# Performance work log

Measured on AMD Instinct MI355X. Metric: run time of the kernel, lower is better.

## Reference

```python
import jax, jax.numpy as jnp
import numpy as np

C = 256
CI = C // 2  # inter_channels


def conv1x1(x, w, b):
    # x: [B,C,H,W], w: [O,C], b: [O] -> [B,O,H,W]
    return jnp.einsum('bchw,oc->bohw', x, w) + b[None, :, None, None]


def setup_inputs() -> dict:
    key = jax.random.key(0)
    ks = jax.random.split(key, 9)
    B, H, W = 8, 56, 56
    s = 0.02
    return {
        'x': jax.random.normal(ks[0], (B, C, H, W), dtype=jnp.float32),
        'g_w': jax.random.normal(ks[1], (CI, C), dtype=jnp.float32) * s,
        'g_b': jax.random.normal(ks[2], (CI,), dtype=jnp.float32) * s,
        'theta_w': jax.random.normal(ks[3], (CI, C), dtype=jnp.float32) * s,
        'theta_b': jax.random.normal(ks[4], (CI,), dtype=jnp.float32) * s,
        'phi_w': jax.random.normal(ks[5], (CI, C), dtype=jnp.float32) * s,
        'phi_b': jax.random.normal(ks[6], (CI,), dtype=jnp.float32) * s,
        'W_w': jax.random.normal(ks[7], (C, CI), dtype=jnp.float32) * s,
        'W_b': jax.random.normal(ks[8], (C,), dtype=jnp.float32) * s,
    }


def reference(x, g_w, g_b, theta_w, theta_b, phi_w, phi_b, W_w, W_b):
    B, Cc, H, Wd = x.shape
    N = H * Wd
    g_x = conv1x1(x, g_w, g_b).reshape(B, CI, N).transpose(0, 2, 1)        # [B,N,CI]
    theta_x = conv1x1(x, theta_w, theta_b).reshape(B, CI, N).transpose(0, 2, 1)  # [B,N,CI]
    phi_x = conv1x1(x, phi_w, phi_b).reshape(B, CI, N)                     # [B,CI,N]
    f = jnp.einsum('bnc,bcm->bnm', theta_x, phi_x)                         # [B,N,N]
    attn = jax.nn.softmax(f, axis=-1)
    y = jnp.einsum('bnm,bmc->bnc', attn, g_x)                              # [B,N,CI]
    y = y.transpose(0, 2, 1).reshape(B, CI, H, Wd)                         # [B,CI,H,W]
    z = conv1x1(y, W_w, W_b) + x
    return z
```

## Files before the change

### kernel.cpp

```cpp
#include <hip/hip_runtime.h>

#define NB 8
#define C 256
#define CI 128
#define NPIX 3136
#define NT 64
#define NTILES 49
#define NGQ 13
#define NROWT 98
#define NSPLIT 4
#define LOG2E 1.44269504f

typedef unsigned short u16;
typedef unsigned int u32;
typedef __bf16 bf16x8 __attribute__((ext_vector_type(8)));
typedef float f32x4 __attribute__((ext_vector_type(4)));
typedef float f32x16 __attribute__((ext_vector_type(16)));

static __device__ __forceinline__ u16 f2b(float f) {
  union { float f; u32 u; } v; v.f = f;
  u32 r = v.u + 0x7FFFu + ((v.u >> 16) & 1u);
  return (u16)(r >> 16);
}
static __device__ __forceinline__ float b2f(u16 v) {
  union { u32 u; float f; } x; x.u = ((u32)v) << 16; return x.f;
}
static __device__ __forceinline__ u32 cvtpk(float lo, float hi) {
  u32 r;
  asm("v_cvt_pk_bf16_f32 %0, %1, %2" : "=v"(r) : "v"(lo), "v"(hi));
  return r;
}
static __device__ __forceinline__ void swap32(u32& x, u32& y) {
  asm("v_permlane32_swap_b32 %0, %1" : "+v"(x), "+v"(y));
}
static __device__ __forceinline__ void gl16(const void* g, void* l) {
  __builtin_amdgcn_global_load_lds(
      (const __attribute__((address_space(1))) u32*)g,
      (__attribute__((address_space(3))) u32*)l, 16, 0, 0);
}

__global__ __launch_bounds__(256) void k0_convert(
    const float* __restrict__ g_w, const float* __restrict__ th_w,
    const float* __restrict__ ph_w, const float* __restrict__ W_w,
    u16* __restrict__ wcat, u16* __restrict__ Wbf) {
  int i = blockIdx.x * 256 + threadIdx.x;
  if (i < 98304) {
    int o = i >> 8, c = i & 255;
    float v = (o < 128) ? g_w[o * 256 + c]
            : (o < 256) ? th_w[(o - 128) * 256 + c] * LOG2E
                        : ph_w[(o - 256) * 256 + c];
    wcat[i] = f2b(v);
  } else {
    int j = i - 98304;
    Wbf[j] = f2b(W_w[j]);
  }
}

__global__ __launch_bounds__(256) void k1_proj(
    const float* __restrict__ x, const float* __restrict__ g_b,
    const float* __restrict__ th_b, const float* __restrict__ ph_b,
    const u16* __restrict__ wcat, u16* __restrict__ thO,
    u16* __restrict__ phO, u16* __restrict__ gO) {
  __shared__ __align__(16) u16 xT[32 * 256];
  char* xTb = reinterpret_cast<char*>(xT);
  int tid = threadIdx.x;
  int b = blockIdx.x / NROWT, nt = blockIdx.x % NROWT;
  int n0 = nt * 32;
  const float* xb = x + (size_t)b * C * NPIX;
  {
    int c0 = tid >> 3, nq = tid & 7;
    for (int k = 0; k < 8; ++k) {
      int c = c0 + 32 * k;
      float4 xv = *reinterpret_cast<const float4*>(xb + (size_t)c * NPIX + n0 + 4 * nq);
      float vals[4] = {xv.x, xv.y, xv.z, xv.w};
#pragma unroll
      for (int j = 0; j < 4; ++j) {
        int row = 4 * nq + j;
        int off = row * 512 + ((((c >> 3) ^ (row & 7))) << 4) + (c & 7) * 2;
        *reinterpret_cast<u16*>(xTb + off) = f2b(vals[j]);
      }
    }
  }
  __syncthreads();
  int wave = tid >> 6, lane = tid & 63;
  int wq = wave & 1, wo = wave >> 1;
  int r = 16 * wq + (lane & 15);
  bf16x8 a[8];
#pragma unroll
  for (int kk = 0; kk < 8; ++kk) {
    int ch = 4 * kk + (lane >> 4);
    a[kk] = *reinterpret_cast<const bf16x8*>(xTb + r * 512 + ((ch ^ (r & 7)) << 4));
  }
  for (int os = 12 * wo; os < 12 * wo + 12; ++os) {
    int o = 16 * os + (lane & 15);
    f32x4 acc = {0.f, 0.f, 0.f, 0.f};
    const u16* wrow = wcat + (size_t)o * 256 + 8 * (lane >> 4);
#pragma unroll
    for (int kk = 0; kk < 8; ++kk) {
      bf16x8 bb = *reinterpret_cast<const bf16x8*>(wrow + 32 * kk);
      acc = __builtin_amdgcn_mfma_f32_16x16x32_bf16(a[kk], bb, acc, 0, 0, 0);
    }
    int p = os >> 3;
    int ol = (os & 7) * 16 + (lane & 15);
    const float* bias = (p == 0) ? g_b : (p == 1) ? th_b : ph_b;
    float bv = bias[ol];
    if (p == 1) bv *= LOG2E;
    int nbase = n0 + 16 * wq + 4 * (lane >> 4);
    if (p == 0) {
      ushort4 pk;
      pk.x = f2b(acc[0] + bv); pk.y = f2b(acc[1] + bv);
      pk.z = f2b(acc[2] + bv); pk.w = f2b(acc[3] + bv);
      *reinterpret_cast<ushort4*>(gO + ((size_t)b * CI + ol) * NPIX + nbase) = pk;
    } else {
      u16* dst = (p == 1) ? thO : phO;
#pragma unroll
      for (int j = 0; j < 4; ++j)
        dst[((size_t)b * NPIX + nbase + j) * CI + ol] = f2b(acc[j] + bv);
    }
  }
}

__global__ __launch_bounds__(512, 2) void k2_attn(
    const u16* __restrict__ th, const u16* __restrict__ ph,
    const u16* __restrict__ gbuf, u16* __restrict__ yp,
    float* __restrict__ lm) {
  __shared__ __align__(16) char lds[65536];
  int tid = threadIdx.x, wave = tid >> 6, lane = tid & 63;
  int h5 = lane >> 5, l31 = lane & 31;
  int bid = blockIdx.x;
  int s = bid & 3, rest = bid >> 2;
  int b = rest / NGQ, ng = rest % NGQ;
  int qbase = ng * 256 + wave * 32;
  if (qbase + 32 > NPIX) qbase = NPIX - 32;
  int ts = (NTILES * s) >> 2, te = (NTILES * (s + 1)) >> 2;

  bf16x8 bth[8];
  {
    const u16* trow = th + ((size_t)b * NPIX + qbase + l31) * CI;
#pragma unroll
    for (int ks = 0; ks < 8; ++ks)
      bth[ks] = *reinterpret_cast<const bf16x8*>(trow + 16 * ks + 8 * h5);
  }
  float lrun = 0.f;
  f32x16 yacc[4];
#pragma unroll
  for (int cb = 0; cb < 4; ++cb)
#pragma unroll
    for (int j = 0; j < 16; ++j) yacc[cb][j] = 0.f;

  auto stage = [&](int buf, int mt) {
    int m0 = mt * NT;
    char* phB = lds + buf * 16384;
    char* gB = lds + 32768 + buf * 16384;
#pragma unroll
    for (int c = 0; c < 2; ++c) {
      int call = wave * 2 + c;
      int o = call * 1024 + lane * 16;
      int row = o >> 8, chl = (o >> 4) & 15;
      int chg = chl ^ (row & 15);
      gl16(ph + ((size_t)(b * NPIX + m0 + row)) * CI + chg * 8, phB + call * 1024);
    }
#pragma unroll
    for (int c = 0; c < 2; ++c) {
      int call = wave * 2 + c;
      int o = call * 1024 + lane * 16;
      int ci = o >> 7, chl = (o >> 4) & 7;
      int chg = chl ^ (ci & 7);
      gl16(gbuf + ((size_t)b * CI + ci) * NPIX + m0 + chg * 8, gB + call * 1024);
    }
  };

  stage(0, ts);
  int cur = 0;
  for (int mt = ts; mt < te; ++mt) {
    bool pre = (mt + 1 < te);
    if (pre) stage(cur ^ 1, mt + 1);
    if (pre) {
      asm volatile("s_waitcnt vmcnt(4)" ::: "memory");
    } else {
      asm volatile("s_waitcnt vmcnt(0)" ::: "memory");
    }
    __builtin_amdgcn_s_barrier();
    __builtin_amdgcn_sched_barrier(0);
    char* phB = lds + cur * 16384;
    char* gB = lds + 32768 + cur * 16384;
    f32x16 sv0, sv1;
#pragma unroll
    for (int j = 0; j < 16; ++j) { sv0[j] = 0.f; sv1[j] = 0.f; }
    __builtin_amdgcn_s_setprio(1);
#pragma unroll
    for (int ks = 0; ks < 8; ++ks) {
      int chk = 2 * ks + h5;
      int off = l31 * 256 + ((chk ^ (l31 & 15)) << 4);
      bf16x8 a0 = *reinterpret_cast<const bf16x8*>(phB + off);
      bf16x8 a1 = *reinterpret_cast<const bf16x8*>(phB + off + 8192);
      sv0 = __builtin_amdgcn_mfma_f32_32x32x16_bf16(a0, bth[ks], sv0, 0, 0, 0);
      sv1 = __builtin_amdgcn_mfma_f32_32x32x16_bf16(a1, bth[ks], sv1, 0, 0, 0);
    }
    __builtin_amdgcn_s_setprio(0);
#pragma unroll
    for (int j = 0; j < 16; ++j) {
      sv0[j] = exp2f(sv0[j]);
      sv1[j] = exp2f(sv1[j]);
    }
    float a0 = 0.f, a1 = 0.f, a2 = 0.f, a3 = 0.f;
#pragma unroll
    for (int i = 0; i < 16; i += 4) {
      a0 += sv0[i] + sv1[i];
      a1 += sv0[i + 1] + sv1[i + 1];
      a2 += sv0[i + 2] + sv1[i + 2];
      a3 += sv0[i + 3] + sv1[i + 3];
    }
    lrun += (a0 + a1) + (a2 + a3);
    u32 pk[2][4][2];
#pragma unroll
    for (int t = 0; t < 4; ++t) {
      pk[0][t][0] = cvtpk(sv0[4 * t], sv0[4 * t + 1]);
      pk[0][t][1] = cvtpk(sv0[4 * t + 2], sv0[4 * t + 3]);
      pk[1][t][0] = cvtpk(sv1[4 * t], sv1[4 * t + 1]);
      pk[1][t][1] = cvtpk(sv1[4 * t + 2], sv1[4 * t + 3]);
    }
    __builtin_amdgcn_s_setprio(1);
#pragma unroll
    for (int ks = 0; ks < 4; ++ks) {
      int m2 = ks >> 1, t0 = 2 * (ks & 1);
      swap32(pk[m2][t0][0], pk[m2][t0 + 1][0]);
      swap32(pk[m2][t0][1], pk[m2][t0 + 1][1]);
      union { u32 u[4]; bf16x8 v; } f;
      f.u[0] = pk[m2][t0][0]; f.u[1] = pk[m2][t0][1];
      f.u[2] = pk[m2][t0 + 1][0]; f.u[3] = pk[m2][t0 + 1][1];
      int chk = 2 * ks + h5;
#pragma unroll
      for (int cb = 0; cb < 4; ++cb) {
        int ci = 32 * cb + l31;
        bf16x8 gv = *reinterpret_cast<const bf16x8*>(
            gB + ci * 128 + ((chk ^ (ci & 7)) << 4));
        yacc[cb] = __builtin_amdgcn_mfma_f32_32x32x16_bf16(f.v, gv, yacc[cb], 0, 0, 0);
      }
    }
    __builtin_amdgcn_s_setprio(0);
    __builtin_amdgcn_sched_barrier(0);
    asm volatile("s_waitcnt lgkmcnt(0)" ::: "memory");
    __builtin_amdgcn_s_barrier();
    cur ^= 1;
  }
  lrun += __shfl_xor(lrun, 32);
  u16* ypb = yp + (size_t)(s * NB + b) * NPIX * CI;
#pragma unroll
  for (int cb = 0; cb < 4; ++cb)
#pragma unroll
    for (int j = 0; j < 16; ++j) {
      int n = qbase + (j & 3) + 8 * (j >> 2) + 4 * h5;
      ypb[(size_t)n * CI + 32 * cb + l31] = f2b(yacc[cb][j]);
    }
  if (lane < 32) {
    int n = qbase + l31;
    lm[(size_t)(s * NB + b) * NPIX + n] = lrun;
  }
}

__global__ __launch_bounds__(256) void k3_out(
    const u16* __restrict__ yp, const float* __restrict__ lm,
    const u16* __restrict__ Wbf, const float* __restrict__ W_b,
    const float* __restrict__ x, float* __restrict__ z) {
  __shared__ __align__(16) u16 yT[32 * 128];
  char* yTb = reinterpret_cast<char*>(yT);
  int tid = threadIdx.x, wave = tid >> 6, lane = tid & 63;
  int b = blockIdx.x / NROWT, nt = blockIdx.x % NROWT;
  int n0 = nt * 32;
#pragma unroll
  for (int i = 0; i < 2; ++i) {
    int qq = tid + i * 256;
    int row = qq >> 4, ch = qq & 15;
    int n = n0 + row;
    float den = 0.f;
    float num[8];
#pragma unroll
    for (int e = 0; e < 8; ++e) num[e] = 0.f;
#pragma unroll
    for (int s = 0; s < NSPLIT; ++s) {
      den += lm[(size_t)(s * NB + b) * NPIX + n];
      union { uint4 u4; u16 us[8]; } yv;
      yv.u4 = *reinterpret_cast<const uint4*>(
          yp + (size_t)(s * NB + b) * NPIX * CI + (size_t)n * CI + ch * 8);
#pragma unroll
      for (int e = 0; e < 8; ++e) num[e] += b2f(yv.us[e]);
    }
    float inv = 1.f / den;
    union { uint4 u4; u16 us[8]; } ov;
#pragma unroll
    for (int e = 0; e < 8; ++e) ov.us[e] = f2b(num[e] * inv);
    *reinterpret_cast<uint4*>(yTb + row * 256 + ((ch ^ (row & 7)) << 4)) = ov.u4;
  }
  __syncthreads();
  int wq = wave & 1, wo = wave >> 1;
  bf16x8 a[4];
  int r = 16 * wq + (lane & 15);
#pragma unroll
  for (int kk = 0; kk < 4; ++kk) {
    int ch = 4 * kk + (lane >> 4);
    a[kk] = *reinterpret_cast<const bf16x8*>(yTb + r * 256 + ((ch ^ (r & 7)) << 4));
  }
  for (int os = 8 * wo; os < 8 * wo + 8; ++os) {
    int co = 16 * os + (lane & 15);
    f32x4 acc = {0.f, 0.f, 0.f, 0.f};
    const u16* wrow = Wbf + (size_t)co * 128 + 8 * (lane >> 4);
#pragma unroll
    for (int kk = 0; kk < 4; ++kk) {
      bf16x8 bb = *reinterpret_cast<const bf16x8*>(wrow + 32 * kk);
      acc = __builtin_amdgcn_mfma_f32_16x16x32_bf16(a[kk], bb, acc, 0, 0, 0);
    }
    float bw = W_b[co];
    int nb = n0 + 16 * wq + 4 * (lane >> 4);
    size_t off = ((size_t)b * C + co) * NPIX + nb;
    float4 xv = *reinterpret_cast<const float4*>(x + off);
    float4 o;
    o.x = acc[0] + bw + xv.x; o.y = acc[1] + bw + xv.y;
    o.z = acc[2] + bw + xv.z; o.w = acc[3] + bw + xv.w;
    *reinterpret_cast<float4*>(z + off) = o;
  }
}

extern "C" void kernel_launch(void* const* d_in, const int* in_sizes, int n_in,
                              void* d_out, int out_size, void* d_ws, size_t ws_size,
                              hipStream_t stream) {
  const float* x    = (const float*)d_in[0];
  const float* g_w  = (const float*)d_in[1];
  const float* g_b  = (const float*)d_in[2];
  const float* th_w = (const float*)d_in[3];
  const float* th_b = (const float*)d_in[4];
  const float* ph_w = (const float*)d_in[5];
  const float* ph_b = (const float*)d_in[6];
  const float* W_w  = (const float*)d_in[7];
  const float* W_b  = (const float*)d_in[8];
  float* z = (float*)d_out;
  u16* ws = (u16*)d_ws;
  u16* wcat = ws;
  u16* Wbf  = ws + 98304;
  u16* th   = ws + 131072;
  u16* phb  = th + 3211264;
  u16* gbb  = phb + 3211264;
  u16* yp   = gbb + 3211264;
  float* lm = (float*)(ws + 131072 + (size_t)3211264 * 7);
  hipLaunchKernelGGL(k0_convert, dim3(512), dim3(256), 0, stream,
                     g_w, th_w, ph_w, W_w, wcat, Wbf);
  hipLaunchKernelGGL(k1_proj, dim3(NB * NROWT), dim3(256), 0, stream,
                     x, g_b, th_b, ph_b, wcat, th, phb, gbb);
  hipLaunchKernelGGL(k2_attn, dim3(NB * NGQ * NSPLIT), dim3(512), 0, stream,
                     th, phb, gbb, yp, lm);
  hipLaunchKernelGGL(k3_out, dim3(NB * NROWT), dim3(256), 0, stream,
                     yp, lm, Wbf, W_b, x, z);
}
```

Measured before the change: 147.5 us.

## Pad LDS rows instead of XOR swizzle and swap MFMA operands in output kernel

The projection and output kernels drop the XOR-swizzled LDS layout and use padded row strides (264 and 136 elements) instead, which simplifies address arithmetic while still avoiding bank conflicts. In the attention kernel the first MFMA of each tile now takes a zero accumulator directly, so the per-tile zeroing of the score registers goes away. The output kernel swaps its MFMA operands so each lane owns one pixel and four output channels. It then writes z and reads x with scalar accesses that are coalesced across pixels, replacing the float4 accesses strided by channel. The scalar global accesses may cost more instructions than the old vectorized ones.

```diff
diff --git a/kernel.cpp b/kernel.cpp
--- a/kernel.cpp
+++ b/kernel.cpp
@@ -61,7 +61,7 @@
     const float* __restrict__ th_b, const float* __restrict__ ph_b,
     const u16* __restrict__ wcat, u16* __restrict__ thO,
     u16* __restrict__ phO, u16* __restrict__ gO) {
-  __shared__ __align__(16) u16 xT[32 * 256];
+  __shared__ __align__(16) u16 xT[32 * 264];
   char* xTb = reinterpret_cast<char*>(xT);
   int tid = threadIdx.x;
   int b = blockIdx.x / NROWT, nt = blockIdx.x % NROWT;
@@ -76,8 +76,7 @@
 #pragma unroll
       for (int j = 0; j < 4; ++j) {
         int row = 4 * nq + j;
-        int off = row * 512 + ((((c >> 3) ^ (row & 7))) << 4) + (c & 7) * 2;
-        *reinterpret_cast<u16*>(xTb + off) = f2b(vals[j]);
+        xT[row * 264 + c] = f2b(vals[j]);
       }
     }
   }
@@ -89,7 +88,7 @@
 #pragma unroll
   for (int kk = 0; kk < 8; ++kk) {
     int ch = 4 * kk + (lane >> 4);
-    a[kk] = *reinterpret_cast<const bf16x8*>(xTb + r * 512 + ((ch ^ (r & 7)) << 4));
+    a[kk] = *reinterpret_cast<const bf16x8*>(xTb + r * 528 + ch * 16);
   }
   for (int os = 12 * wo; os < 12 * wo + 12; ++os) {
     int o = 16 * os + (lane & 15);
@@ -142,6 +141,9 @@
       bth[ks] = *reinterpret_cast<const bf16x8*>(trow + 16 * ks + 8 * h5);
   }
   float lrun = 0.f;
+  f32x16 zv;
+#pragma unroll
+  for (int j = 0; j < 16; ++j) zv[j] = 0.f;
   f32x16 yacc[4];
 #pragma unroll
   for (int cb = 0; cb < 4; ++cb)
@@ -185,11 +187,16 @@
     char* phB = lds + cur * 16384;
     char* gB = lds + 32768 + cur * 16384;
     f32x16 sv0, sv1;
-#pragma unroll
-    for (int j = 0; j < 16; ++j) { sv0[j] = 0.f; sv1[j] = 0.f; }
     __builtin_amdgcn_s_setprio(1);
-#pragma unroll
-    for (int ks = 0; ks < 8; ++ks) {
+    {
+      int off = l31 * 256 + ((h5 ^ (l31 & 15)) << 4);
+      bf16x8 a0 = *reinterpret_cast<const bf16x8*>(phB + off);
+      bf16x8 a1 = *reinterpret_cast<const bf16x8*>(phB + off + 8192);
+      sv0 = __builtin_amdgcn_mfma_f32_32x32x16_bf16(a0, bth[0], zv, 0, 0, 0);
+      sv1 = __builtin_amdgcn_mfma_f32_32x32x16_bf16(a1, bth[0], zv, 0, 0, 0);
+    }
+#pragma unroll
+    for (int ks = 1; ks < 8; ++ks) {
       int chk = 2 * ks + h5;
       int off = l31 * 256 + ((chk ^ (l31 & 15)) << 4);
       bf16x8 a0 = *reinterpret_cast<const bf16x8*>(phB + off);
@@ -263,8 +270,7 @@
     const u16* __restrict__ yp, const float* __restrict__ lm,
     const u16* __restrict__ Wbf, const float* __restrict__ W_b,
     const float* __restrict__ x, float* __restrict__ z) {
-  __shared__ __align__(16) u16 yT[32 * 128];
-  char* yTb = reinterpret_cast<char*>(yT);
+  __shared__ __align__(16) u16 yT[32 * 136];
   int tid = threadIdx.x, wave = tid >> 6, lane = tid & 63;
   int b = blockIdx.x / NROWT, nt = blockIdx.x % NROWT;
   int n0 = nt * 32;
@@ -290,34 +296,31 @@
     union { uint4 u4; u16 us[8]; } ov;
 #pragma unroll
     for (int e = 0; e < 8; ++e) ov.us[e] = f2b(num[e] * inv);
-    *reinterpret_cast<uint4*>(yTb + row * 256 + ((ch ^ (row & 7)) << 4)) = ov.u4;
+    *reinterpret_cast<uint4*>(yT + row * 136 + ch * 8) = ov.u4;
   }
   __syncthreads();
+  int q = lane >> 4, l15 = lane & 15;
   int wq = wave & 1, wo = wave >> 1;
-  bf16x8 a[4];
-  int r = 16 * wq + (lane & 15);
-#pragma unroll
-  for (int kk = 0; kk < 4; ++kk) {
-    int ch = 4 * kk + (lane >> 4);
-    a[kk] = *reinterpret_cast<const bf16x8*>(yTb + r * 256 + ((ch ^ (r & 7)) << 4));
-  }
+  int n = n0 + 16 * wq + l15;
+  bf16x8 bf[4];
+#pragma unroll
+  for (int kk = 0; kk < 4; ++kk)
+    bf[kk] = *reinterpret_cast<const bf16x8*>(yT + (16 * wq + l15) * 136 + 32 * kk + 8 * q);
   for (int os = 8 * wo; os < 8 * wo + 8; ++os) {
-    int co = 16 * os + (lane & 15);
     f32x4 acc = {0.f, 0.f, 0.f, 0.f};
-    const u16* wrow = Wbf + (size_t)co * 128 + 8 * (lane >> 4);
+    const u16* wrow = Wbf + (size_t)(16 * os + l15) * 128 + 8 * q;
 #pragma unroll
     for (int kk = 0; kk < 4; ++kk) {
-      bf16x8 bb = *reinterpret_cast<const bf16x8*>(wrow + 32 * kk);
-      acc = __builtin_amdgcn_mfma_f32_16x16x32_bf16(a[kk], bb, acc, 0, 0, 0);
-    }
-    float bw = W_b[co];
-    int nb = n0 + 16 * wq + 4 * (lane >> 4);
-    size_t off = ((size_t)b * C + co) * NPIX + nb;
-    float4 xv = *reinterpret_cast<const float4*>(x + off);
-    float4 o;
-    o.x = acc[0] + bw + xv.x; o.y = acc[1] + bw + xv.y;
-    o.z = acc[2] + bw + xv.z; o.w = acc[3] + bw + xv.w;
-    *reinterpret_cast<float4*>(z + off) = o;
+      bf16x8 aw = *reinterpret_cast<const bf16x8*>(wrow + 32 * kk);
+      acc = __builtin_amdgcn_mfma_f32_16x16x32_bf16(aw, bf[kk], acc, 0, 0, 0);
+    }
+    float4 bwv = *reinterpret_cast<const float4*>(W_b + 16 * os + 4 * q);
+    float bw[4] = {bwv.x, bwv.y, bwv.z, bwv.w};
+#pragma unroll
+    for (int j = 0; j < 4; ++j) {
+      size_t off = ((size_t)b * C + 16 * os + 4 * q + j) * NPIX + n;
+      z[off] = acc[j] + bw[j] + x[off];
+    }
   }
 }
 
```

Measured after the change: 152.6 us. 3.5% more time.
